# Performance work log

Hardware: AMD Instinct MI355X
Metric: run time of the kernel (lower is better)

Reference implementation:

```python
import jax, jax.numpy as jnp
import numpy as np

B, C, CI, H, W = 4, 256, 128, 64, 64  # batch, in_channels, inter_channels, spatial


def setup_inputs() -> dict:
    key = jax.random.key(0)
    ks = jax.random.split(key, 9)
    p = lambda k, shape: jax.random.normal(k, shape, jnp.float32) * 0.05
    return {
        "x": jax.random.normal(ks[0], (B, C, H, W), jnp.float32),
        "g_w": p(ks[1], (CI, C)), "g_b": p(ks[2], (CI,)),
        "theta_w": p(ks[3], (CI, C)), "theta_b": p(ks[4], (CI,)),
        "phi_w": p(ks[5], (CI, C)), "phi_b": p(ks[6], (CI,)),
        "out_w": p(ks[7], (C, CI)), "out_b": p(ks[8], (C,)),
    }


def reference(x, g_w, g_b, theta_w, theta_b, phi_w, phi_b, out_w, out_b):
    n, c, h, w = x.shape
    xf = x.reshape(n, c, h * w)  # (b, C, N)
    # 1x1 convs as channel matmuls
    g_x = jnp.einsum('bcn,oc->bno', xf, g_w) + g_b              # (b, N, CI)
    theta_x = jnp.einsum('bcn,oc->bno', xf, theta_w) + theta_b  # (b, N, CI)
    phi_x = jnp.einsum('bcn,oc->bon', xf, phi_w) + phi_b[:, None]  # (b, CI, N)
    # 'channel' whitening: theta centered over channel axis per position,
    # phi centered over spatial axis per channel (as in source)
    theta_x = theta_x - theta_x.mean(axis=2, keepdims=True)
    phi_x = phi_x - phi_x.mean(axis=2, keepdims=True)
    # no softmax / no scaling in this forward
    pairwise = jnp.einsum('bnc,bcm->bnm', theta_x, phi_x)  # (b, N, N)
    y = jnp.einsum('bnm,bmc->bnc', pairwise, g_x)          # (b, N, CI)
    out = jnp.einsum('bnc,oc->bon', y, out_w) + out_b[:, None]  # (b, C, N)
    return x + out.reshape(n, c, h, w)
```

## Files before the change

kernel.cpp:

```cpp
#include <hip/hip_runtime.h>

constexpr int kB  = 4;
constexpr int kC  = 256;
constexpr int kCI = 128;
constexpr int kN  = 64 * 64;


constexpr int kSplits = 64;

typedef __attribute__((ext_vector_type(8))) short bf16x8;
typedef __attribute__((ext_vector_type(4))) float f32x4;

__device__ inline ushort f2b(float f) {
    unsigned u = __float_as_uint(f);
    return (ushort)((u + 0x7FFF + ((u >> 16) & 1)) >> 16);
}

constexpr long kOffTwcT  = 0;
constexpr long kOffTbc   = kOffTwcT + kC * kCI;
constexpr long kOffPG    = kOffTbc + kCI;
constexpr long kOffRs    = kOffPG + (long)kB * kC * kN;
constexpr long kOffTpart = kOffRs + kB * kC;
constexpr long kOffT     = kOffTpart + (long)kB * kSplits * kCI * kCI;
constexpr long kOffW2t   = kOffT + kB * kCI * kCI;
constexpr long kOffMt    = kOffW2t + kB * kC * kCI;
constexpr long kOffBeta  = kOffMt + kB * kC * kC;
constexpr long kOffXT    = kOffBeta + kB * kC;

__global__ void __launch_bounds__(256, 4)
xt_kernel(const float* __restrict__ x, ushort* __restrict__ xT) {
    int b = blockIdx.z;
    int n0 = blockIdx.x * 64, c0 = blockIdx.y * 64;
    __shared__ float ft[64][66];
    int t = threadIdx.x;
    const float* xb = x + (long)b * kC * kN;
#pragma unroll
    for (int i = 0; i < 4; i++) {
        int l = t + 256 * i;
        int row = l >> 4, col4 = (l & 15) * 4;
        float4 v = *(const float4*)(xb + (long)(c0 + row) * kN + n0 + col4);
        ft[row][col4 + 0] = v.x; ft[row][col4 + 1] = v.y;
        ft[row][col4 + 2] = v.z; ft[row][col4 + 3] = v.w;
    }
    __syncthreads();
    {
        int n = t >> 2, cs = (t & 3) * 16;
        unsigned w[8];
#pragma unroll
        for (int j = 0; j < 8; j++) {
            ushort lo = f2b(ft[cs + 2 * j][n]);
            ushort hi = f2b(ft[cs + 2 * j + 1][n]);
            w[j] = (unsigned)lo | ((unsigned)hi << 16);
        }
        ushort* dst = xT + ((long)b * kN + n0 + n) * kC + c0 + cs;
        ((uint4*)dst)[0] = make_uint4(w[0], w[1], w[2], w[3]);
        ((uint4*)dst)[1] = make_uint4(w[4], w[5], w[6], w[7]);
    }
}

__global__ void centerw_kernel(const float* __restrict__ theta_w,
                               const float* __restrict__ theta_b,
                               float* __restrict__ twcT, float* __restrict__ tbc) {
    __shared__ float sm[128];
    int t = threadIdx.x;
    if (t < 128) sm[t] = theta_b[t];
    __syncthreads();
    for (int st = 64; st > 0; st >>= 1) {
        if (t < st) sm[t] += sm[t + st];
        __syncthreads();
    }
    float bmean = sm[0] * (1.f / kCI);
    float m = 0.f;
    for (int k = 0; k < kCI; k++) m += theta_w[k * kC + t];
    m *= (1.f / kCI);
    for (int k = 0; k < kCI; k++) twcT[t * kCI + k] = theta_w[k * kC + t] - m;
    if (t < 128) tbc[t] = theta_b[t] - bmean;
}

__global__ void __launch_bounds__(256, 2)
pg_mfma(const float* __restrict__ phi_w, const float* __restrict__ g_w,
        const ushort* __restrict__ xT, float* __restrict__ PG) {
    int b = blockIdx.z;
    int r0 = blockIdx.y * 128, n0 = blockIdx.x * 64;
    const float* wbase = blockIdx.y == 0 ? phi_w : g_w;
    __shared__ ushort Ws[128 * 40];
    __shared__ ushort Xs[64 * 40];
    int t = threadIdx.x;
    int w = t >> 6, lane = t & 63, q = lane >> 4, ln = lane & 15;
    f32x4 acc[2][4];
#pragma unroll
    for (int i = 0; i < 2; i++)
#pragma unroll
        for (int j = 0; j < 4; j++) acc[i][j] = 0.f;
    const ushort* xTb = xT + ((long)b * kN + n0) * kC;
    for (int kc = 0; kc < kC; kc += 32) {
        __syncthreads();
#pragma unroll
        for (int it = 0; it < 4; it++) {
            int l = t + 256 * it;
            int row = l >> 3, seg = l & 7;
            float4 v = *(const float4*)(wbase + (long)row * kC + kc + seg * 4);
            ushort4 u = {f2b(v.x), f2b(v.y), f2b(v.z), f2b(v.w)};
            *(ushort4*)&Ws[row * 40 + seg * 4] = u;
        }
        {
            int row = t >> 2, seg = t & 3;
            uint4 v = *(const uint4*)(xTb + (long)row * kC + kc + seg * 8);
            *(uint4*)&Xs[row * 40 + seg * 8] = v;
        }
        __syncthreads();
        bf16x8 a[2], bb[4];
#pragma unroll
        for (int mt = 0; mt < 2; mt++)
            a[mt] = *(const bf16x8*)&Ws[(32 * w + 16 * mt + ln) * 40 + q * 8];
#pragma unroll
        for (int nt = 0; nt < 4; nt++)
            bb[nt] = *(const bf16x8*)&Xs[(16 * nt + ln) * 40 + q * 8];
#pragma unroll
        for (int mt = 0; mt < 2; mt++)
#pragma unroll
            for (int nt = 0; nt < 4; nt++)
                acc[mt][nt] = __builtin_amdgcn_mfma_f32_16x16x32_bf16(
                    a[mt], bb[nt], acc[mt][nt], 0, 0, 0);
    }
    float* pb = PG + (long)b * kC * kN;
#pragma unroll
    for (int mt = 0; mt < 2; mt++)
#pragma unroll
        for (int nt = 0; nt < 4; nt++)
#pragma unroll
            for (int i = 0; i < 4; i++) {
                int row = r0 + 32 * w + 16 * mt + 4 * q + i;
                int col = n0 + 16 * nt + ln;
                pb[(long)row * kN + col] = acc[mt][nt][i];
            }
}

__global__ void rowsum_kernel(const float* __restrict__ PG, float* __restrict__ rs) {
    int br = blockIdx.x;
    const float* p = PG + (long)br * kN;
    float s = 0.f;
    for (int i = threadIdx.x * 4; i < kN; i += 1024) {
        float4 v = *(const float4*)(p + i);
        s += v.x + v.y + v.z + v.w;
    }
    __shared__ float sm[256];
    sm[threadIdx.x] = s;
    __syncthreads();
    for (int st = 128; st > 0; st >>= 1) {
        if (threadIdx.x < st) sm[threadIdx.x] += sm[threadIdx.x + st];
        __syncthreads();
    }
    if (threadIdx.x == 0) rs[br] = sm[0];
}

__global__ void __launch_bounds__(256, 4)
tsplit_kernel(const float* __restrict__ PG, float* __restrict__ Tpart) {
    int s = blockIdx.x, b = blockIdx.z;
    int qy = blockIdx.y >> 1, qx = blockIdx.y & 1;
    int mbase = s * (kN / kSplits);
    __shared__ __align__(16) float As[16][68];
    __shared__ __align__(16) float Bs[16][68];
    int t = threadIdx.x;
    int tx = t & 15, ty = t >> 4;
    float acc[4][4] = {};
    const float* Phi = PG + (long)b * kC * kN + (long)(64 * qy) * kN;
    const float* G2  = PG + (long)b * kC * kN + (long)(kCI + 64 * qx) * kN;
    for (int mc = 0; mc < kN / kSplits; mc += 16) {
        __syncthreads();
        {
            int r = t >> 2, c4 = (t & 3) * 4;
            float4 va = *(const float4*)(Phi + (long)r * kN + mbase + mc + c4);
            As[c4 + 0][r] = va.x; As[c4 + 1][r] = va.y;
            As[c4 + 2][r] = va.z; As[c4 + 3][r] = va.w;
            float4 vb = *(const float4*)(G2 + (long)r * kN + mbase + mc + c4);
            Bs[c4 + 0][r] = vb.x; Bs[c4 + 1][r] = vb.y;
            Bs[c4 + 2][r] = vb.z; Bs[c4 + 3][r] = vb.w;
        }
        __syncthreads();
#pragma unroll
        for (int k = 0; k < 16; k++) {
            float4 a = *(const float4*)&As[k][4 * ty];
            float4 bv = *(const float4*)&Bs[k][4 * tx];
            float av[4] = {a.x, a.y, a.z, a.w};
            float bw[4] = {bv.x, bv.y, bv.z, bv.w};
#pragma unroll
            for (int i = 0; i < 4; i++)
#pragma unroll
                for (int j = 0; j < 4; j++) acc[i][j] += av[i] * bw[j];
        }
    }
    float* Tp = Tpart + ((long)b * kSplits + s) * kCI * kCI;
#pragma unroll
    for (int i = 0; i < 4; i++) {
        int c = 64 * qy + ty * 4 + i;
        float4 ov = {acc[i][0], acc[i][1], acc[i][2], acc[i][3]};
        *(float4*)(Tp + (long)c * kCI + 64 * qx + tx * 4) = ov;
    }
}

__global__ void treduce_kernel(const float* __restrict__ Tpart, const float* __restrict__ rs,
                               float* __restrict__ T) {
    int idx = blockIdx.x * 256 + threadIdx.x;
    int b = idx >> 14;
    int c = (idx >> 7) & 127, cp = idx & 127;
    const float* tp = Tpart + (long)b * kSplits * kCI * kCI + (idx & 16383);
    float s = 0.f;
#pragma unroll 8
    for (int sl = 0; sl < kSplits; sl++) s += tp[(long)sl * kCI * kCI];
    s -= rs[b * kC + c] * rs[b * kC + kCI + cp] * (1.f / kN);
    T[idx] = s;
}

__global__ void __launch_bounds__(256, 4)
nt64_gemm(const float* __restrict__ A, const float* __restrict__ B,
          float* __restrict__ Cm, int M, int N, int K,
          long sA, long sB, long sC) {
    int b = blockIdx.z;
    const float* Ab = A + (long)b * sA;
    const float* Bb = B + (long)b * sB;
    float* Cb = Cm + (long)b * sC;
    __shared__ __align__(16) float As[16][68];
    __shared__ __align__(16) float Bs[16][68];
    int t = threadIdx.x;
    int tx = t & 15, ty = t >> 4;
    int m0 = blockIdx.y * 64, n0 = blockIdx.x * 64;
    float acc[4][4] = {};
    for (int kc = 0; kc < K; kc += 16) {
        __syncthreads();
        {
            int r = t >> 2, c4 = (t & 3) * 4;
            float4 va = *(const float4*)(Ab + (long)(m0 + r) * K + kc + c4);
            As[c4 + 0][r] = va.x; As[c4 + 1][r] = va.y;
            As[c4 + 2][r] = va.z; As[c4 + 3][r] = va.w;
            float4 vb = *(const float4*)(Bb + (long)(n0 + r) * K + kc + c4);
            Bs[c4 + 0][r] = vb.x; Bs[c4 + 1][r] = vb.y;
            Bs[c4 + 2][r] = vb.z; Bs[c4 + 3][r] = vb.w;
        }
        __syncthreads();
#pragma unroll
        for (int k = 0; k < 16; k++) {
            float4 a = *(const float4*)&As[k][4 * ty];
            float4 bv = *(const float4*)&Bs[k][4 * tx];
            float av[4] = {a.x, a.y, a.z, a.w};
            float bw[4] = {bv.x, bv.y, bv.z, bv.w};
#pragma unroll
            for (int i = 0; i < 4; i++)
#pragma unroll
                for (int j = 0; j < 4; j++) acc[i][j] += av[i] * bw[j];
        }
    }
#pragma unroll
    for (int i = 0; i < 4; i++) {
        float4 ov = {acc[i][0], acc[i][1], acc[i][2], acc[i][3]};
        *(float4*)(Cb + (long)(m0 + 4 * ty + i) * N + n0 + 4 * tx) = ov;
    }
}

__global__ void beta_kernel(const float* __restrict__ W2t, const float* __restrict__ tbc,
                            const float* __restrict__ out_b, float* __restrict__ beta) {
    int i = blockIdx.x * blockDim.x + threadIdx.x;
    if (i >= kB * kC) return;
    int o = i & (kC - 1);
    float s = out_b[o];
    const float* row = W2t + (long)i * kCI;
#pragma unroll 8
    for (int k = 0; k < kCI; k++) s += tbc[k] * row[k];
    beta[i] = s;
}

__global__ void __launch_bounds__(256, 2)
final_mfma(const float* __restrict__ x, const float* __restrict__ Mt,
           const ushort* __restrict__ xT, const float* __restrict__ beta,
           float* __restrict__ out) {
    int b = blockIdx.z;
    int o0 = blockIdx.y * 128, n0 = blockIdx.x * 64;
    const float* Mb = Mt + (long)b * kC * kC;
    __shared__ ushort Ws[128 * 40];
    __shared__ ushort Xs[64 * 40];
    int t = threadIdx.x;
    int w = t >> 6, lane = t & 63, q = lane >> 4, ln = lane & 15;
    f32x4 acc[2][4];
#pragma unroll
    for (int i = 0; i < 2; i++)
#pragma unroll
        for (int j = 0; j < 4; j++) acc[i][j] = 0.f;
    const ushort* xTb = xT + ((long)b * kN + n0) * kC;
    for (int kc = 0; kc < kC; kc += 32) {
        __syncthreads();
#pragma unroll
        for (int it = 0; it < 4; it++) {
            int l = t + 256 * it;
            int row = l >> 3, seg = l & 7;
            float4 v = *(const float4*)(Mb + (long)(o0 + row) * kC + kc + seg * 4);
            ushort4 u = {f2b(v.x), f2b(v.y), f2b(v.z), f2b(v.w)};
            *(ushort4*)&Ws[row * 40 + seg * 4] = u;
        }
        {
            int row = t >> 2, seg = t & 3;
            uint4 v = *(const uint4*)(xTb + (long)row * kC + kc + seg * 8);
            *(uint4*)&Xs[row * 40 + seg * 8] = v;
        }
        __syncthreads();
        bf16x8 a[2], bb[4];
#pragma unroll
        for (int mt = 0; mt < 2; mt++)
            a[mt] = *(const bf16x8*)&Ws[(32 * w + 16 * mt + ln) * 40 + q * 8];
#pragma unroll
        for (int nt = 0; nt < 4; nt++)
            bb[nt] = *(const bf16x8*)&Xs[(16 * nt + ln) * 40 + q * 8];
#pragma unroll
        for (int mt = 0; mt < 2; mt++)
#pragma unroll
            for (int nt = 0; nt < 4; nt++)
                acc[mt][nt] = __builtin_amdgcn_mfma_f32_16x16x32_bf16(
                    a[mt], bb[nt], acc[mt][nt], 0, 0, 0);
    }
    const float* xb = x + (long)b * kC * kN;
    float* ob = out + (long)b * kC * kN;
#pragma unroll
    for (int mt = 0; mt < 2; mt++)
#pragma unroll
        for (int nt = 0; nt < 4; nt++)
#pragma unroll
            for (int i = 0; i < 4; i++) {
                int row = o0 + 32 * w + 16 * mt + 4 * q + i;
                int col = n0 + 16 * nt + ln;
                long idx = (long)row * kN + col;
                ob[idx] = acc[mt][nt][i] + xb[idx] + beta[b * kC + row];
            }
}

extern "C" void kernel_launch(void* const* d_in, const int* in_sizes, int n_in,
                              void* d_out, int out_size, void* d_ws, size_t ws_size,
                              hipStream_t stream) {
    const float* x       = (const float*)d_in[0];
    const float* g_w     = (const float*)d_in[1];
    const float* theta_w = (const float*)d_in[3];
    const float* theta_b = (const float*)d_in[4];
    const float* phi_w   = (const float*)d_in[5];
    const float* out_w   = (const float*)d_in[7];
    const float* out_b   = (const float*)d_in[8];
    float* out = (float*)d_out;
    float* ws  = (float*)d_ws;

    float*  twcT  = ws + kOffTwcT;
    float*  tbc   = ws + kOffTbc;
    float*  PG    = ws + kOffPG;
    float*  rs    = ws + kOffRs;
    float*  Tpart = ws + kOffTpart;
    float*  T     = ws + kOffT;
    float*  W2t   = ws + kOffW2t;
    float*  Mt    = ws + kOffMt;
    float*  beta  = ws + kOffBeta;
    ushort* xT    = (ushort*)(ws + kOffXT);

    xt_kernel<<<dim3(kN / 64, kC / 64, kB), 256, 0, stream>>>(x, xT);
    centerw_kernel<<<1, 256, 0, stream>>>(theta_w, theta_b, twcT, tbc);
    pg_mfma<<<dim3(kN / 64, 2, kB), 256, 0, stream>>>(phi_w, g_w, xT, PG);
    rowsum_kernel<<<kB * kC, 256, 0, stream>>>(PG, rs);
    tsplit_kernel<<<dim3(kSplits, 4, kB), 256, 0, stream>>>(PG, Tpart);
    treduce_kernel<<<kB * kCI * kCI / 256, 256, 0, stream>>>(Tpart, rs, T);
    nt64_gemm<<<dim3(2, 4, kB), 256, 0, stream>>>(out_w, T, W2t, kC, kCI, kCI,
                                                  0, (long)kCI * kCI, (long)kC * kCI);
    nt64_gemm<<<dim3(4, 4, kB), 256, 0, stream>>>(W2t, twcT, Mt, kC, kC, kCI,
                                                  (long)kC * kCI, 0, (long)kC * kC);
    beta_kernel<<<kB, 256, 0, stream>>>(W2t, tbc, out_b, beta);
    final_mfma<<<dim3(kN / 64, 2, kB), 256, 0, stream>>>(x, Mt, xT, beta, out);
}
```

Before: 159.8 us.

## Store phi/g projections as bf16 and compute split T with MFMA

The phi/g projection buffer is now written in bf16 instead of fp32, halving its write and read traffic. The split-N reduction that builds phi·gᵀ moves from a scalar fp32 FMA kernel to bf16 MFMA tiles. The split count drops from 64 to 16, shrinking the partial buffer and the reduce pass. This trades accuracy for speed: the long reduction over N now uses bf16-rounded inputs, and the fewer splits give less parallelism in the T stage.

```diff
diff --git a/kernel.cpp b/kernel.cpp
--- a/kernel.cpp
+++ b/kernel.cpp
@@ -6,7 +6,8 @@
 constexpr int kN  = 64 * 64;
 
 
-constexpr int kSplits = 64;
+constexpr int kSplits = 16;
+constexpr int kSliceN = kN / kSplits;
 
 typedef __attribute__((ext_vector_type(8))) short bf16x8;
 typedef __attribute__((ext_vector_type(4))) float f32x4;
@@ -15,11 +16,12 @@
     unsigned u = __float_as_uint(f);
     return (ushort)((u + 0x7FFF + ((u >> 16) & 1)) >> 16);
 }
+__device__ inline float b2f(ushort u) { return __uint_as_float((unsigned)u << 16); }
 
 constexpr long kOffTwcT  = 0;
 constexpr long kOffTbc   = kOffTwcT + kC * kCI;
 constexpr long kOffPG    = kOffTbc + kCI;
-constexpr long kOffRs    = kOffPG + (long)kB * kC * kN;
+constexpr long kOffRs    = kOffPG + (long)kB * kC * kN / 2;
 constexpr long kOffTpart = kOffRs + kB * kC;
 constexpr long kOffT     = kOffTpart + (long)kB * kSplits * kCI * kCI;
 constexpr long kOffW2t   = kOffT + kB * kCI * kCI;
@@ -79,7 +81,7 @@
 
 __global__ void __launch_bounds__(256, 2)
 pg_mfma(const float* __restrict__ phi_w, const float* __restrict__ g_w,
-        const ushort* __restrict__ xT, float* __restrict__ PG) {
+        const ushort* __restrict__ xT, ushort* __restrict__ PGh) {
     int b = blockIdx.z;
     int r0 = blockIdx.y * 128, n0 = blockIdx.x * 64;
     const float* wbase = blockIdx.y == 0 ? phi_w : g_w;
@@ -123,7 +125,7 @@
                 acc[mt][nt] = __builtin_amdgcn_mfma_f32_16x16x32_bf16(
                     a[mt], bb[nt], acc[mt][nt], 0, 0, 0);
     }
-    float* pb = PG + (long)b * kC * kN;
+    ushort* pb = PGh + (long)b * kC * kN;
 #pragma unroll
     for (int mt = 0; mt < 2; mt++)
 #pragma unroll
@@ -132,17 +134,22 @@
             for (int i = 0; i < 4; i++) {
                 int row = r0 + 32 * w + 16 * mt + 4 * q + i;
                 int col = n0 + 16 * nt + ln;
-                pb[(long)row * kN + col] = acc[mt][nt][i];
+                pb[(long)row * kN + col] = f2b(acc[mt][nt][i]);
             }
 }
 
-__global__ void rowsum_kernel(const float* __restrict__ PG, float* __restrict__ rs) {
+__global__ void rowsum_kernel(const ushort* __restrict__ PGh, float* __restrict__ rs) {
     int br = blockIdx.x;
-    const float* p = PG + (long)br * kN;
+    const ushort* p = PGh + (long)br * kN;
     float s = 0.f;
-    for (int i = threadIdx.x * 4; i < kN; i += 1024) {
-        float4 v = *(const float4*)(p + i);
-        s += v.x + v.y + v.z + v.w;
+    for (int i = threadIdx.x * 8; i < kN; i += 2048) {
+        uint4 v = *(const uint4*)(p + i);
+        unsigned ww[4] = {v.x, v.y, v.z, v.w};
+#pragma unroll
+        for (int j = 0; j < 4; j++) {
+            s += __uint_as_float(ww[j] << 16);
+            s += __uint_as_float(ww[j] & 0xFFFF0000u);
+        }
     }
     __shared__ float sm[256];
     sm[threadIdx.x] = s;
@@ -155,48 +162,45 @@
 }
 
 __global__ void __launch_bounds__(256, 4)
-tsplit_kernel(const float* __restrict__ PG, float* __restrict__ Tpart) {
+tsplit_mfma(const ushort* __restrict__ PGh, float* __restrict__ Tpart) {
     int s = blockIdx.x, b = blockIdx.z;
     int qy = blockIdx.y >> 1, qx = blockIdx.y & 1;
-    int mbase = s * (kN / kSplits);
-    __shared__ __align__(16) float As[16][68];
-    __shared__ __align__(16) float Bs[16][68];
-    int t = threadIdx.x;
-    int tx = t & 15, ty = t >> 4;
-    float acc[4][4] = {};
-    const float* Phi = PG + (long)b * kC * kN + (long)(64 * qy) * kN;
-    const float* G2  = PG + (long)b * kC * kN + (long)(kCI + 64 * qx) * kN;
-    for (int mc = 0; mc < kN / kSplits; mc += 16) {
+    long nbase = (long)s * kSliceN;
+    __shared__ ushort As[64 * 40];
+    __shared__ ushort Bs[64 * 40];
+    int t = threadIdx.x;
+    int w = t >> 6, lane = t & 63, q = lane >> 4, ln = lane & 15;
+    f32x4 acc[4];
+#pragma unroll
+    for (int j = 0; j < 4; j++) acc[j] = 0.f;
+    const ushort* Phi = PGh + ((long)b * kC + 64 * qy) * kN + nbase;
+    const ushort* G2  = PGh + ((long)b * kC + kCI + 64 * qx) * kN + nbase;
+    for (int kc = 0; kc < kSliceN; kc += 32) {
         __syncthreads();
         {
-            int r = t >> 2, c4 = (t & 3) * 4;
-            float4 va = *(const float4*)(Phi + (long)r * kN + mbase + mc + c4);
-            As[c4 + 0][r] = va.x; As[c4 + 1][r] = va.y;
-            As[c4 + 2][r] = va.z; As[c4 + 3][r] = va.w;
-            float4 vb = *(const float4*)(G2 + (long)r * kN + mbase + mc + c4);
-            Bs[c4 + 0][r] = vb.x; Bs[c4 + 1][r] = vb.y;
-            Bs[c4 + 2][r] = vb.z; Bs[c4 + 3][r] = vb.w;
-        }
-        __syncthreads();
-#pragma unroll
-        for (int k = 0; k < 16; k++) {
-            float4 a = *(const float4*)&As[k][4 * ty];
-            float4 bv = *(const float4*)&Bs[k][4 * tx];
-            float av[4] = {a.x, a.y, a.z, a.w};
-            float bw[4] = {bv.x, bv.y, bv.z, bv.w};
-#pragma unroll
-            for (int i = 0; i < 4; i++)
-#pragma unroll
-                for (int j = 0; j < 4; j++) acc[i][j] += av[i] * bw[j];
+            int row = t >> 2, seg = t & 3;
+            *(uint4*)&As[row * 40 + seg * 8] =
+                *(const uint4*)(Phi + (long)row * kN + kc + seg * 8);
+            *(uint4*)&Bs[row * 40 + seg * 8] =
+                *(const uint4*)(G2 + (long)row * kN + kc + seg * 8);
+        }
+        __syncthreads();
+        bf16x8 a = *(const bf16x8*)&As[(16 * w + ln) * 40 + q * 8];
+#pragma unroll
+        for (int nt = 0; nt < 4; nt++) {
+            bf16x8 bb = *(const bf16x8*)&Bs[(16 * nt + ln) * 40 + q * 8];
+            acc[nt] = __builtin_amdgcn_mfma_f32_16x16x32_bf16(a, bb, acc[nt], 0, 0, 0);
         }
     }
     float* Tp = Tpart + ((long)b * kSplits + s) * kCI * kCI;
 #pragma unroll
-    for (int i = 0; i < 4; i++) {
-        int c = 64 * qy + ty * 4 + i;
-        float4 ov = {acc[i][0], acc[i][1], acc[i][2], acc[i][3]};
-        *(float4*)(Tp + (long)c * kCI + 64 * qx + tx * 4) = ov;
-    }
+    for (int nt = 0; nt < 4; nt++)
+#pragma unroll
+        for (int i = 0; i < 4; i++) {
+            int c  = 64 * qy + 16 * w + 4 * q + i;
+            int cp = 64 * qx + 16 * nt + ln;
+            Tp[(long)c * kCI + cp] = acc[nt][i];
+        }
 }
 
 __global__ void treduce_kernel(const float* __restrict__ Tpart, const float* __restrict__ rs,
@@ -206,7 +210,7 @@
     int c = (idx >> 7) & 127, cp = idx & 127;
     const float* tp = Tpart + (long)b * kSplits * kCI * kCI + (idx & 16383);
     float s = 0.f;
-#pragma unroll 8
+#pragma unroll
     for (int sl = 0; sl < kSplits; sl++) s += tp[(long)sl * kCI * kCI];
     s -= rs[b * kC + c] * rs[b * kC + kCI + cp] * (1.f / kN);
     T[idx] = s;
@@ -346,7 +350,7 @@
 
     float*  twcT  = ws + kOffTwcT;
     float*  tbc   = ws + kOffTbc;
-    float*  PG    = ws + kOffPG;
+    ushort* PGh   = (ushort*)(ws + kOffPG);
     float*  rs    = ws + kOffRs;
     float*  Tpart = ws + kOffTpart;
     float*  T     = ws + kOffT;
@@ -357,9 +361,9 @@
 
     xt_kernel<<<dim3(kN / 64, kC / 64, kB), 256, 0, stream>>>(x, xT);
     centerw_kernel<<<1, 256, 0, stream>>>(theta_w, theta_b, twcT, tbc);
-    pg_mfma<<<dim3(kN / 64, 2, kB), 256, 0, stream>>>(phi_w, g_w, xT, PG);
-    rowsum_kernel<<<kB * kC, 256, 0, stream>>>(PG, rs);
-    tsplit_kernel<<<dim3(kSplits, 4, kB), 256, 0, stream>>>(PG, Tpart);
+    pg_mfma<<<dim3(kN / 64, 2, kB), 256, 0, stream>>>(phi_w, g_w, xT, PGh);
+    rowsum_kernel<<<kB * kC, 256, 0, stream>>>(PGh, rs);
+    tsplit_mfma<<<dim3(kSplits, 4, kB), 256, 0, stream>>>(PGh, Tpart);
     treduce_kernel<<<kB * kCI * kCI / 256, 256, 0, stream>>>(Tpart, rs, T);
     nt64_gemm<<<dim3(2, 4, kB), 256, 0, stream>>>(out_w, T, W2t, kC, kCI, kCI,
                                                   0, (long)kCI * kCI, (long)kC * kCI);
```

Result: faster. 151.0 us (-5.5%).
